# Kernel tuning notes

Hardware: AMD Instinct MI355X
Metric: run time of the kernel (lower is better)

The kernel has to match this reference:

```python
import jax, jax.numpy as jnp
import numpy as np

IMG = 224          # mask height/width, hardcoded in the module
OUT = 256          # Linear(224*224 -> 256)
BOX = 20           # half-width of the square mask around the farthest joint


def setup_inputs() -> dict:
    key = jax.random.key(0)
    k1, k2, k3, k4 = jax.random.split(key, 4)
    B, J, T = 256, 25, 64
    rgbfuture = jax.random.normal(k1, (B, OUT), dtype=jnp.float32)
    # normalized joint coords kept in [0.1, 0.9] so pixel_x in [22, 201] (original
    # code has no x-clamping and would hit numpy negative-slice wraparound otherwise)
    skeleton_future = 0.1 + 0.8 * jax.random.uniform(k2, (B, J, T, 3), dtype=jnp.float32)
    W = jax.random.normal(k3, (OUT, IMG * IMG), dtype=jnp.float32) / np.sqrt(IMG * IMG)
    b = jax.random.normal(k4, (OUT,), dtype=jnp.float32) * 0.01
    return {"rgbfuture": rgbfuture, "skeleton_future": skeleton_future, "W": W, "b": b}


def reference(rgbfuture, skeleton_future, W, b):
    B, J, T, _ = skeleton_future.shape
    mid = J // 2

    # distance of every joint trajectory to the middle joint, per frame: [B, J, T]
    diff = skeleton_future - skeleton_future[:, mid:mid + 1]
    dist = jnp.linalg.norm(diff, axis=-1)
    t_max = jnp.argmax(dist, axis=-1)                       # [B, J]

    # farthest-frame coordinates per joint: [B, J, 3]
    pts = jnp.take_along_axis(skeleton_future, t_max[:, :, None, None], axis=2)[:, :, 0, :]
    px = (pts[..., 0] * IMG).astype(jnp.int32)              # int() truncation == floor (positive)
    py = (pts[..., 1] * IMG).astype(jnp.int32)

    rows = jnp.arange(IMG)
    # x-range: [px-20, px+20) (inputs guarantee in-frame)
    xm = (rows >= (px - BOX)[..., None]) & (rows < (px + BOX)[..., None])   # [B, J, IMG]
    # y-range with the module's explicit edge handling
    y_lo = jnp.where(py < BOX, 0, py - BOX)
    y_hi = jnp.where(py > IMG - BOX, IMG, py + BOX)
    ym = (rows >= y_lo[..., None]) & (rows < y_hi[..., None])               # [B, J, IMG]

    keep = jnp.arange(J) != mid                              # middle joint is skipped
    box = xm[:, :, :, None] & ym[:, :, None, :] & keep[None, :, None, None]  # [B, J, IMG, IMG]
    mask = jnp.any(box, axis=1).astype(rgbfuture.dtype)      # torch.max over joints == union

    merged = mask.reshape(B, IMG * IMG) @ W.T + b            # [B, 256]
    return rgbfuture * merged
```

## Files before the change

### kernel.cpp

```cpp
#include <hip/hip_runtime.h>
#include <hip/hip_bf16.h>
#include <stdint.h>

#define IMG   224
#define OUTD  256
#define BATCH 256
#define JD    25
#define TD    64
#define MIDJ  12
#define BOXR  20
#define NSL   16
#define SLW   14

typedef float vfloat4 __attribute__((ext_vector_type(4)));

#define OFF_EV   25804800u
#define OFF_EVC  29999104u
#define OFF_PART 30015488u


__global__ void KA(const float* __restrict__ W, __hip_bfloat16* __restrict__ P,
                   const float* __restrict__ skel, uint32_t* __restrict__ evlist,
                   uint32_t* __restrict__ evcnt) {
    const int id  = blockIdx.x;
    const int tid = threadIdx.x;

    __shared__ float lds[64][225];
    __shared__ float carry[8][64];
    __shared__ int s_px[JD], s_ylo[JD], s_yhi[JD];
    __shared__ uint32_t s_n[IMG];

    if (id < 896) {
        const int xcd = id & 7;
        const int r   = id >> 3;
        const int oc  = r & 3;
        const int q   = r >> 2;
        const int xi  = q % 14;
        const int hi8 = q / 14;
        const int x   = (hi8 * 8 + xcd) * SLW + xi;
        const int o0  = oc * 64;

        #pragma unroll
        for (int it = 0; it < 7; ++it) {
            const int k = it * 512 + tid;
            const int rr = k / 56;
            const int c  = k - rr * 56;
            const vfloat4 v = __builtin_nontemporal_load(
                (const vfloat4*)&W[(size_t)(o0 + rr) * (IMG * IMG) + (size_t)x * IMG + c * 4]);
            lds[rr][c * 4 + 0] = v.x;
            lds[rr][c * 4 + 1] = v.y;
            lds[rr][c * 4 + 2] = v.z;
            lds[rr][c * 4 + 3] = v.w;
        }
        __syncthreads();

        const int ol  = tid & 63;
        const int seg = tid >> 6;
        const int y0  = seg * 28;

        float rv[28];
        #pragma unroll
        for (int i = 0; i < 28; ++i) rv[i] = lds[ol][y0 + i];

        float ssum = 0.0f;
        #pragma unroll
        for (int i = 0; i < 28; ++i) ssum += rv[i];
        carry[seg][ol] = ssum;
        __syncthreads();

        float s = 0.0f;
        for (int s2 = 0; s2 < seg; ++s2) s += carry[s2][ol];

        __hip_bfloat16* p = P + ((size_t)x * 225) * 256 + o0 + ol;
        if (seg == 0) p[0] = __float2bfloat16(0.0f);
        #pragma unroll
        for (int i = 0; i < 28; ++i) {
            s += rv[i];
            p[(size_t)(y0 + i + 1) * 256] = __float2bfloat16(s);
        }
        return;
    }

    const int b = id - 896;
    const int wave = tid >> 6;
    const int t = tid & 63;

    const float* sb = skel + (size_t)b * JD * TD * 3;
    const float mx = sb[(MIDJ * TD + t) * 3 + 0];
    const float my = sb[(MIDJ * TD + t) * 3 + 1];
    const float mz = sb[(MIDJ * TD + t) * 3 + 2];

    for (int j = wave; j < JD; j += 8) {
        const float ax = sb[(j * TD + t) * 3 + 0];
        const float ay = sb[(j * TD + t) * 3 + 1];
        const float az = sb[(j * TD + t) * 3 + 2];
        const float dx = ax - mx, dy = ay - my, dz = az - mz;
        const float d2 = __fadd_rn(__fadd_rn(__fmul_rn(dx, dx), __fmul_rn(dy, dy)),
                                   __fmul_rn(dz, dz));
        float bd = sqrtf(d2);
        int   bi = t;
        #pragma unroll
        for (int off = 1; off < 64; off <<= 1) {
            const float od = __shfl_xor(bd, off);
            const int   oi = __shfl_xor(bi, off);
            if (od > bd || (od == bd && oi < bi)) { bd = od; bi = oi; }
        }
        if (t == 0) {
            const float ptx = sb[(j * TD + bi) * 3 + 0];
            const float pty = sb[(j * TD + bi) * 3 + 1];
            const int px = (int)(ptx * 224.0f);
            const int py = (int)(pty * 224.0f);
            s_px[j]  = px;
            s_ylo[j] = (py < BOXR) ? 0 : (py - BOXR);
            s_yhi[j] = (py > IMG - BOXR) ? IMG : (py + BOXR);
        }
    }
    __syncthreads();

    const int x = tid;
    unsigned long long m0 = 0, m1 = 0, m2 = 0, m3 = 0;
    uint32_t n = 0;
    if (x < IMG) {
        for (int j = 0; j < JD; ++j) {
            if (j == MIDJ) continue;
            const int px = s_px[j];
            if (x >= px - BOXR && x < px + BOXR) {
                const int lo = s_ylo[j], hi = s_yhi[j];
                auto setw = [&](unsigned long long& mw, int wbase) {
                    int l = lo - wbase; int h = hi - wbase;
                    l = l < 0 ? 0 : l; h = h > 64 ? 64 : h;
                    if (l < h) {
                        unsigned long long msk =
                            (h - l == 64) ? ~0ull : ((((1ull << (h - l)) - 1ull)) << l);
                        mw |= msk;
                    }
                };
                setw(m0, 0); setw(m1, 64); setw(m2, 128); setw(m3, 192);
            }
        }
        const unsigned long long e0 = m0 & ~(m0 << 1);
        const unsigned long long e1 = m1 & ~((m1 << 1) | (m0 >> 63));
        const unsigned long long e2 = m2 & ~((m2 << 1) | (m1 >> 63));
        const unsigned long long e3 = m3 & ~((m3 << 1) | (m2 >> 63));
        n = (uint32_t)(__popcll(e0) + __popcll(e1) + __popcll(e2) + __popcll(e3));
        s_n[x] = n;
    }
    __syncthreads();
    if (x >= IMG) return;

    const int sl = x / SLW;
    const int xl = x - sl * SLW;
    uint32_t off = 0;
    for (int i = sl * SLW; i < x; ++i) off += s_n[i];
    if (xl == SLW - 1) evcnt[(size_t)b * NSL + sl] = off + n;

    uint32_t* evs = evlist + ((size_t)b * NSL + sl) * 256 + off;
    int k = 0, start = -1;
    auto scanw = [&](unsigned long long bits, int wbase) {
        int pos = 0;
        while (pos < 64) {
            if (start < 0) {
                const unsigned long long tt = bits >> pos;
                if (!tt) return;
                pos += __builtin_ctzll(tt);
                start = wbase + pos;
            } else {
                const unsigned long long tt = (~bits) >> pos;
                if (!tt) return;
                pos += __builtin_ctzll(tt);
                evs[k] = (uint32_t)xl | ((uint32_t)start << 5)
                                      | ((uint32_t)(wbase + pos) << 13);
                ++k; start = -1;
            }
        }
    };
    scanw(m0, 0); scanw(m1, 64); scanw(m2, 128); scanw(m3, 192);
    if (start >= 0) { evs[k] = (uint32_t)xl | ((uint32_t)start << 5) | (224u << 13); }
}

__global__ void k_accum(const uint32_t* __restrict__ evlist,
                        const uint32_t* __restrict__ evcnt,
                        const uint32_t* __restrict__ P32,
                        float* __restrict__ part) {
    const int bs  = blockIdx.x;
    const int s   = bs & (NSL - 1);
    const int tid = threadIdx.x;
    const int x0  = s * SLW;

    __shared__ uint32_t slist[256];

    const uint32_t cntv = evcnt[bs];
    slist[tid]       = evlist[(size_t)bs * 256 + tid];
    slist[128 + tid] = evlist[(size_t)bs * 256 + 128 + tid];
    __syncthreads();

    const int total = (int)cntv;
    const uint32_t* Pbase = P32 + (size_t)x0 * (225 * 128) + tid;

    float aLo[8] = {0.f,0.f,0.f,0.f,0.f,0.f,0.f,0.f};
    float aHi[8] = {0.f,0.f,0.f,0.f,0.f,0.f,0.f,0.f};
    int i = 0;
    for (; i + 8 <= total; i += 8) {
        uint32_t ev[8], va[8], vc[8];
        #pragma unroll
        for (int u = 0; u < 8; ++u) ev[u] = slist[i + u];
        #pragma unroll
        for (int u = 0; u < 8; ++u) {
            const uint32_t* p = Pbase + (size_t)(ev[u] & 31u) * (225 * 128);
            va[u] = p[(size_t)((ev[u] >> 5) & 255u) * 128];
            vc[u] = p[(size_t)((ev[u] >> 13) & 255u) * 128];
        }
        #pragma unroll
        for (int u = 0; u < 8; ++u) {
            aLo[u] += __uint_as_float(vc[u] << 16) - __uint_as_float(va[u] << 16);
            aHi[u] += __uint_as_float(vc[u] & 0xffff0000u) - __uint_as_float(va[u] & 0xffff0000u);
        }
    }
    for (; i < total; ++i) {
        const uint32_t e0 = slist[i];
        const uint32_t* p0 = Pbase + (size_t)(e0 & 31u) * (225 * 128);
        const uint32_t va0 = p0[(size_t)((e0 >> 5) & 255u) * 128];
        const uint32_t vc0 = p0[(size_t)((e0 >> 13) & 255u) * 128];
        aLo[0] += __uint_as_float(vc0 << 16) - __uint_as_float(va0 << 16);
        aHi[0] += __uint_as_float(vc0 & 0xffff0000u) - __uint_as_float(va0 & 0xffff0000u);
    }

    const float lo = ((aLo[0] + aLo[1]) + (aLo[2] + aLo[3]))
                   + ((aLo[4] + aLo[5]) + (aLo[6] + aLo[7]));
    const float hi = ((aHi[0] + aHi[1]) + (aHi[2] + aHi[3]))
                   + ((aHi[4] + aHi[5]) + (aHi[6] + aHi[7]));

    float* pp = part + ((size_t)bs * 256) + (size_t)tid * 2;
    pp[0] = lo;
    pp[1] = hi;
}

__global__ void k_final(const float* __restrict__ rgb, const float* __restrict__ bias,
                        const float* __restrict__ part, float* __restrict__ out) {
    const int idx = blockIdx.x * 256 + threadIdx.x;
    const int b = idx >> 8, o = idx & 255;
    float m = bias[o];
    #pragma unroll
    for (int s = 0; s < NSL; ++s) m += part[(((size_t)b * NSL + s) * 256) + o];
    out[idx] = rgb[idx] * m;
}

extern "C" void kernel_launch(void* const* d_in, const int* in_sizes, int n_in,
                              void* d_out, int out_size, void* d_ws, size_t ws_size,
                              hipStream_t stream) {
    const float* rgb  = (const float*)d_in[0];
    const float* skel = (const float*)d_in[1];
    const float* W    = (const float*)d_in[2];
    const float* bias = (const float*)d_in[3];
    float* out = (float*)d_out;

    uint8_t* ws = (uint8_t*)d_ws;
    __hip_bfloat16* P = (__hip_bfloat16*)(ws);
    uint32_t* evlist = (uint32_t*)(ws + OFF_EV);
    uint32_t* evcnt  = (uint32_t*)(ws + OFF_EVC);
    float* part = (float*)(ws + OFF_PART);

    KA<<<dim3(1152), dim3(512), 0, stream>>>(W, P, skel, evlist, evcnt);
    k_accum<<<dim3(BATCH * NSL), dim3(128), 0, stream>>>(evlist, evcnt, (const uint32_t*)P, part);
    k_final<<<dim3(BATCH), dim3(256), 0, stream>>>(rgb, bias, part, out);
}
```

Measured before the change: 40.10 us.

## Fuse accumulation and final epilogue into one per-batch kernel with in-block reduction

Replaces the per-(batch, x-slice) accumulation kernel and the separate final kernel with a single kernel per batch row of 1024 threads. The event list becomes one list per batch, split across 8 thread groups, and the groups are reduced in LDS before bias and the rgb multiply are applied in place. This removes the partial-sum round trip through global memory and one kernel launch. In exchange each block handles more work, the grid shrinks from 4096 blocks to 256, and a fixed cap of 1536 events per batch is assumed.

```diff
diff --git a/kernel.cpp b/kernel.cpp
--- a/kernel.cpp
+++ b/kernel.cpp
@@ -9,14 +9,12 @@
 #define TD    64
 #define MIDJ  12
 #define BOXR  20
-#define NSL   16
-#define SLW   14
+#define MAXEV 1536
 
 typedef float vfloat4 __attribute__((ext_vector_type(4)));
 
 #define OFF_EV   25804800u
-#define OFF_EVC  29999104u
-#define OFF_PART 30015488u
+#define OFF_EVC  27377664u
 
 
 __global__ void KA(const float* __restrict__ W, __hip_bfloat16* __restrict__ P,
@@ -37,12 +35,12 @@
         const int q   = r >> 2;
         const int xi  = q % 14;
         const int hi8 = q / 14;
-        const int x   = (hi8 * 8 + xcd) * SLW + xi;
+        const int x   = (hi8 * 8 + xcd) * 14 + xi;
         const int o0  = oc * 64;
 
         #pragma unroll
         for (int it = 0; it < 7; ++it) {
-            const int k = it * 512 + tid;
+            const int k  = it * 512 + tid;
             const int rr = k / 56;
             const int c  = k - rr * 56;
             const vfloat4 v = __builtin_nontemporal_load(
@@ -148,13 +146,11 @@
     __syncthreads();
     if (x >= IMG) return;
 
-    const int sl = x / SLW;
-    const int xl = x - sl * SLW;
     uint32_t off = 0;
-    for (int i = sl * SLW; i < x; ++i) off += s_n[i];
-    if (xl == SLW - 1) evcnt[(size_t)b * NSL + sl] = off + n;
-
-    uint32_t* evs = evlist + ((size_t)b * NSL + sl) * 256 + off;
+    for (int i = 0; i < x; ++i) off += s_n[i];
+    if (x == IMG - 1) evcnt[b] = off + n;
+
+    uint32_t* evs = evlist + (size_t)b * MAXEV + off;
     int k = 0, start = -1;
     auto scanw = [&](unsigned long long bits, int wbase) {
         int pos = 0;
@@ -168,47 +164,53 @@
                 const unsigned long long tt = (~bits) >> pos;
                 if (!tt) return;
                 pos += __builtin_ctzll(tt);
-                evs[k] = (uint32_t)xl | ((uint32_t)start << 5)
-                                      | ((uint32_t)(wbase + pos) << 13);
+                evs[k] = (uint32_t)x | ((uint32_t)start << 8)
+                                     | ((uint32_t)(wbase + pos) << 16);
                 ++k; start = -1;
             }
         }
     };
     scanw(m0, 0); scanw(m1, 64); scanw(m2, 128); scanw(m3, 192);
-    if (start >= 0) { evs[k] = (uint32_t)xl | ((uint32_t)start << 5) | (224u << 13); }
+    if (start >= 0) { evs[k] = (uint32_t)x | ((uint32_t)start << 8) | (224u << 16); }
 }
 
-__global__ void k_accum(const uint32_t* __restrict__ evlist,
-                        const uint32_t* __restrict__ evcnt,
-                        const uint32_t* __restrict__ P32,
-                        float* __restrict__ part) {
-    const int bs  = blockIdx.x;
-    const int s   = bs & (NSL - 1);
+__global__ void KB(const uint32_t* __restrict__ evlist,
+                   const uint32_t* __restrict__ evcnt,
+                   const uint32_t* __restrict__ P32,
+                   const float* __restrict__ rgb, const float* __restrict__ bias,
+                   float* __restrict__ out) {
+    const int b   = blockIdx.x;
     const int tid = threadIdx.x;
-    const int x0  = s * SLW;
-
-    __shared__ uint32_t slist[256];
-
-    const uint32_t cntv = evcnt[bs];
-    slist[tid]       = evlist[(size_t)bs * 256 + tid];
-    slist[128 + tid] = evlist[(size_t)bs * 256 + 128 + tid];
+    const int g   = tid >> 7;
+    const int l   = tid & 127;
+
+    __shared__ uint32_t slist[MAXEV];
+    __shared__ float sLo[8][128];
+    __shared__ float sHi[8][128];
+
+    const uint32_t cntv = evcnt[b];
+    slist[tid] = evlist[(size_t)b * MAXEV + tid];
+    if (tid < MAXEV - 1024) slist[1024 + tid] = evlist[(size_t)b * MAXEV + 1024 + tid];
     __syncthreads();
 
     const int total = (int)cntv;
-    const uint32_t* Pbase = P32 + (size_t)x0 * (225 * 128) + tid;
-
+    const int chunk = (total + 7) >> 3;
+    const int i0 = g * chunk;
+    const int i1 = min(total, i0 + chunk);
+
+    const uint32_t* Pb = P32 + l;
     float aLo[8] = {0.f,0.f,0.f,0.f,0.f,0.f,0.f,0.f};
     float aHi[8] = {0.f,0.f,0.f,0.f,0.f,0.f,0.f,0.f};
-    int i = 0;
-    for (; i + 8 <= total; i += 8) {
+    int i = i0;
+    for (; i + 8 <= i1; i += 8) {
         uint32_t ev[8], va[8], vc[8];
         #pragma unroll
         for (int u = 0; u < 8; ++u) ev[u] = slist[i + u];
         #pragma unroll
         for (int u = 0; u < 8; ++u) {
-            const uint32_t* p = Pbase + (size_t)(ev[u] & 31u) * (225 * 128);
-            va[u] = p[(size_t)((ev[u] >> 5) & 255u) * 128];
-            vc[u] = p[(size_t)((ev[u] >> 13) & 255u) * 128];
+            const uint32_t* p = Pb + (size_t)(ev[u] & 255u) * (225 * 128);
+            va[u] = p[(size_t)((ev[u] >> 8) & 255u) * 128];
+            vc[u] = p[(size_t)((ev[u] >> 16) & 255u) * 128];
         }
         #pragma unroll
         for (int u = 0; u < 8; ++u) {
@@ -216,33 +218,30 @@
             aHi[u] += __uint_as_float(vc[u] & 0xffff0000u) - __uint_as_float(va[u] & 0xffff0000u);
         }
     }
-    for (; i < total; ++i) {
+    for (; i < i1; ++i) {
         const uint32_t e0 = slist[i];
-        const uint32_t* p0 = Pbase + (size_t)(e0 & 31u) * (225 * 128);
-        const uint32_t va0 = p0[(size_t)((e0 >> 5) & 255u) * 128];
-        const uint32_t vc0 = p0[(size_t)((e0 >> 13) & 255u) * 128];
+        const uint32_t* p0 = Pb + (size_t)(e0 & 255u) * (225 * 128);
+        const uint32_t va0 = p0[(size_t)((e0 >> 8) & 255u) * 128];
+        const uint32_t vc0 = p0[(size_t)((e0 >> 16) & 255u) * 128];
         aLo[0] += __uint_as_float(vc0 << 16) - __uint_as_float(va0 << 16);
         aHi[0] += __uint_as_float(vc0 & 0xffff0000u) - __uint_as_float(va0 & 0xffff0000u);
     }
 
-    const float lo = ((aLo[0] + aLo[1]) + (aLo[2] + aLo[3]))
-                   + ((aLo[4] + aLo[5]) + (aLo[6] + aLo[7]));
-    const float hi = ((aHi[0] + aHi[1]) + (aHi[2] + aHi[3]))
-                   + ((aHi[4] + aHi[5]) + (aHi[6] + aHi[7]));
-
-    float* pp = part + ((size_t)bs * 256) + (size_t)tid * 2;
-    pp[0] = lo;
-    pp[1] = hi;
-}
-
-__global__ void k_final(const float* __restrict__ rgb, const float* __restrict__ bias,
-                        const float* __restrict__ part, float* __restrict__ out) {
-    const int idx = blockIdx.x * 256 + threadIdx.x;
-    const int b = idx >> 8, o = idx & 255;
-    float m = bias[o];
-    #pragma unroll
-    for (int s = 0; s < NSL; ++s) m += part[(((size_t)b * NSL + s) * 256) + o];
-    out[idx] = rgb[idx] * m;
+    sLo[g][l] = ((aLo[0] + aLo[1]) + (aLo[2] + aLo[3]))
+              + ((aLo[4] + aLo[5]) + (aLo[6] + aLo[7]));
+    sHi[g][l] = ((aHi[0] + aHi[1]) + (aHi[2] + aHi[3]))
+              + ((aHi[4] + aHi[5]) + (aHi[6] + aHi[7]));
+    __syncthreads();
+
+    if (tid < 128) {
+        const float lo = ((sLo[0][tid] + sLo[1][tid]) + (sLo[2][tid] + sLo[3][tid]))
+                       + ((sLo[4][tid] + sLo[5][tid]) + (sLo[6][tid] + sLo[7][tid]));
+        const float hi = ((sHi[0][tid] + sHi[1][tid]) + (sHi[2][tid] + sHi[3][tid]))
+                       + ((sHi[4][tid] + sHi[5][tid]) + (sHi[6][tid] + sHi[7][tid]));
+        const size_t o = (size_t)b * 256 + 2 * tid;
+        out[o]     = rgb[o]     * (bias[2 * tid]     + lo);
+        out[o + 1] = rgb[o + 1] * (bias[2 * tid + 1] + hi);
+    }
 }
 
 extern "C" void kernel_launch(void* const* d_in, const int* in_sizes, int n_in,
@@ -258,9 +257,8 @@
     __hip_bfloat16* P = (__hip_bfloat16*)(ws);
     uint32_t* evlist = (uint32_t*)(ws + OFF_EV);
     uint32_t* evcnt  = (uint32_t*)(ws + OFF_EVC);
-    float* part = (float*)(ws + OFF_PART);
 
     KA<<<dim3(1152), dim3(512), 0, stream>>>(W, P, skel, evlist, evcnt);
-    k_accum<<<dim3(BATCH * NSL), dim3(128), 0, stream>>>(evlist, evcnt, (const uint32_t*)P, part);
-    k_final<<<dim3(BATCH), dim3(256), 0, stream>>>(rgb, bias, part, out);
+    KB<<<dim3(BATCH), dim3(1024), 0, stream>>>(evlist, evcnt, (const uint32_t*)P,
+                                               rgb, bias, out);
 }
```

Result: slower. 45.87 us (+14.4%).
